# Kernel tuning notes

Measured on AMD Instinct MI355X. Metric: run time of the kernel, lower is better.

Reference implementation:

```python
import jax, jax.numpy as jnp
import numpy as np

DIM = 1024
HEADS = 16
HEAD_DIM = DIM // HEADS  # 64


def get_rope_matrix(seq_len: int, dim: int) -> jnp.ndarray:
    # rope[s, d] = concat(cos(s * inv_freq), sin(s * inv_freq))  -> (seq_len, dim)
    half = dim // 2
    inv_freq = 1.0 / (10000.0 ** (jnp.arange(half, dtype=jnp.float32) / half))
    sinusoid = jnp.arange(seq_len, dtype=jnp.float32)[:, None] * inv_freq[None, :]
    return jnp.concatenate([jnp.cos(sinusoid), jnp.sin(sinusoid)], axis=-1)


def setup_inputs() -> dict:
    key = jax.random.key(0)
    ks = jax.random.split(key, 6)
    B, T, D = 2, 2048, DIM
    scale = 1.0 / np.sqrt(D)
    return {
        "x": jax.random.normal(ks[0], (B, T, D), dtype=jnp.float32),
        "Wq": jax.random.normal(ks[1], (D, D), dtype=jnp.float32) * scale,
        "Wk": jax.random.normal(ks[2], (D, D), dtype=jnp.float32) * scale,
        "Wv": jax.random.normal(ks[3], (D, D), dtype=jnp.float32) * scale,
        "Wo": jax.random.normal(ks[4], (D, D), dtype=jnp.float32) * scale,
        "bo": jax.random.normal(ks[5], (D,), dtype=jnp.float32) * 0.01,
    }


def reference(x, Wq, Wk, Wv, Wo, bo):
    B, T, D = x.shape
    H, hd = HEADS, HEAD_DIM

    # projections -> (B, H, T, hd)
    def split_heads(y):
        return y.reshape(B, T, H, hd).transpose(0, 2, 1, 3)

    q = split_heads(x @ Wq)
    k = split_heads(x @ Wk)
    v = split_heads(x @ Wv)

    rope = get_rope_matrix(T, hd)  # (T, hd)

    # apply_rope(v, rope): einsum('...nd,sd->...ns') contracts head_dim -> (B,H,T,T)
    v_r = jnp.einsum('bhnd,sd->bhns', v, rope)

    scores = jax.nn.softmax(jnp.einsum('bhnd,bhmd->bhnm', q, k) / jnp.sqrt(jnp.float32(hd)), axis=-1)
    out = jnp.einsum('bhnm,bhms->bhns', scores, v_r)  # (B,H,T,T)

    # apply_rope(out, rope.T): out2[...,n,s] = sum_t out[...,n,t] * rope[t,s] -> (B,H,T,hd)
    out = jnp.einsum('bhnt,ts->bhns', out, rope)

    out = out.transpose(0, 2, 1, 3).reshape(B, T, D)
    return out @ Wo + bo
```

## Files before the change

kernel.cpp:

```cpp
#include <hip/hip_runtime.h>
#include <math.h>

#define DIM 1024
#define NH 16
#define HD 64
#define TT 2048
#define NTOK 4096

typedef __bf16 bf8v __attribute__((ext_vector_type(8)));
typedef float f4v __attribute__((ext_vector_type(4)));
typedef float f16v __attribute__((ext_vector_type(16)));
typedef unsigned short us8 __attribute__((ext_vector_type(8)));
typedef unsigned short us4 __attribute__((ext_vector_type(4)));
typedef unsigned int u4v __attribute__((ext_vector_type(4)));

static __device__ __forceinline__ unsigned short f2bf(float f) {
    unsigned int u = __float_as_uint(f);
    u += 0x7FFFu + ((u >> 16) & 1u);
    return (unsigned short)(u >> 16);
}
static __device__ __forceinline__ bf8v ld8(const unsigned short* p) {
    return __builtin_bit_cast(bf8v, *(const us8*)p);
}
static __device__ __forceinline__ void gl_lds(const unsigned short* g, unsigned short* l) {
    __builtin_amdgcn_global_load_lds((const __attribute__((address_space(1))) unsigned int*)(g),
                                     (__attribute__((address_space(3))) unsigned int*)(l), 16, 0, 0);
}

__global__ void k_prep(const float* __restrict__ x, unsigned short* __restrict__ xb,
                       const float* __restrict__ Wq, const float* __restrict__ Wk,
                       const float* __restrict__ Wv, unsigned short* __restrict__ wt,
                       float* __restrict__ rope, float* __restrict__ Rm) {
    int tid = threadIdx.x;
    int bb = blockIdx.x;
    if (bb < 4096) {
        int i = bb * 256 + tid;
        float4 v = ((const float4*)x)[i];
        us4 o;
        o[0] = f2bf(v.x); o[1] = f2bf(v.y); o[2] = f2bf(v.z); o[3] = f2bf(v.w);
        *(us4*)&xb[i * 4] = o;
    } else if (bb < 7168) {
        __shared__ float tile[32][33];
        bb -= 4096;
        int z = bb >> 10, rem = bb & 1023;
        int bx = rem & 31, by = rem >> 5;
        const float* W = (z == 0) ? Wq : ((z == 1) ? Wk : Wv);
        int tx = tid & 31, ty = tid >> 5;
        int c0 = bx * 32, k0 = by * 32;
#pragma unroll
        for (int j = 0; j < 4; j++)
            tile[ty + j * 8][tx] = W[(k0 + ty + j * 8) * DIM + c0 + tx];
        __syncthreads();
        unsigned short* out = wt + z * DIM * DIM;
#pragma unroll
        for (int j = 0; j < 4; j++)
            out[(c0 + ty + j * 8) * DIM + k0 + tx] = f2bf(tile[tx][ty + j * 8]);
    } else if (bb < 7680) {
        int i = (bb - 7168) * 256 + tid;
        int s = i >> 6, d = i & 63;
        float inv = exp2f(-(float)(d & 31) * (13.287712379549449f / 32.0f));
        float a = (float)s * inv;
        rope[i] = (d < 32) ? cosf(a) : sinf(a);
    } else {
        Rm[(bb - 7680) * 256 + tid] = 0.f;
    }
}

__global__ void k_R(const float* __restrict__ rope, float* __restrict__ R) {
    __shared__ float red[256];
    int d = blockIdx.x & 63, sg = blockIdx.x >> 6;
    int e = threadIdx.x & 63, sl = threadIdx.x >> 6;
    const float* rp = rope + (sg * 256 + sl * 64) * 64;
    float acc = 0.f;
    for (int s = 0; s < 64; s++)
        acc += rp[s * 64 + d] * rp[s * 64 + e];
    red[threadIdx.x] = acc;
    __syncthreads();
    if (sl == 0)
        atomicAdd(&R[d * 64 + e], (red[e] + red[e + 64]) + (red[e + 128] + red[e + 192]));
}

__global__ void k_wo2(const float* __restrict__ Wo, const float* __restrict__ R,
                      unsigned short* __restrict__ wo2t) {
    __shared__ float Ws[64 * 65];
    __shared__ float Rt[64 * 65];
    int tid = threadIdx.x;
    int h = blockIdx.y, j0 = blockIdx.x * 64;
    for (int idx = tid; idx < 4096; idx += 256) {
        int e = idx >> 6, j = idx & 63;
        Ws[e * 65 + j] = Wo[(h * 64 + e) * DIM + j0 + j];
        Rt[e * 65 + j] = R[j * 64 + e];
    }
    __syncthreads();
    int d = tid & 63, jb = (tid >> 6) * 16;
    float acc[16] = {};
    for (int e = 0; e < 64; e++) {
        float r = Rt[e * 65 + d];
#pragma unroll
        for (int jj = 0; jj < 16; jj++)
            acc[jj] += r * Ws[e * 65 + jb + jj];
    }
#pragma unroll
    for (int jj = 0; jj < 16; jj++)
        wo2t[(j0 + jb + jj) * DIM + h * 64 + d] = f2bf(acc[jj]);
}


__global__ __launch_bounds__(256, 3) void k_gemm_qkv(const unsigned short* __restrict__ A,
                                                     const unsigned short* __restrict__ Bt,
                                                     unsigned short* __restrict__ qk,
                                                     unsigned short* __restrict__ vt) {
    __shared__ unsigned short As[128 * 32];
    __shared__ unsigned short Bs[128 * 32];
    const int K = 1024;
    int tid = threadIdx.x;
    int lane = tid & 63, w = tid >> 6;
    int quad = lane >> 4, l16 = lane & 15;
    int m0 = blockIdx.y * 128, n0 = blockIdx.x * 128;
    int wm = (w >> 1) * 64, wn = (w & 1) * 64;

    int s0 = tid, s1 = 256 + tid;
    int r0 = s0 >> 2, cc0 = ((s0 & 3) ^ (r0 & 3)) * 8;
    int r1 = s1 >> 2, cc1 = ((s1 & 3) ^ (r1 & 3)) * 8;
    const unsigned short* Ag0 = A + (m0 + r0) * K + cc0;
    const unsigned short* Ag1 = A + (m0 + r1) * K + cc1;
    const unsigned short* Bg0 = Bt + (n0 + r0) * K + cc0;
    const unsigned short* Bg1 = Bt + (n0 + r1) * K + cc1;
    int qx = quad ^ (l16 & 3);

    f4v acc[4][4] = {};
    for (int k0 = 0; k0 < K; k0 += 32) {
        __syncthreads();
        gl_lds(Ag0 + k0, &As[s0 * 8]);
        gl_lds(Ag1 + k0, &As[s1 * 8]);
        gl_lds(Bg0 + k0, &Bs[s0 * 8]);
        gl_lds(Bg1 + k0, &Bs[s1 * 8]);
        __syncthreads();
        bf8v af[4], bf[4];
#pragma unroll
        for (int mt = 0; mt < 4; mt++)
            af[mt] = ld8(&As[(wm + mt * 16 + l16) * 32 + qx * 8]);
#pragma unroll
        for (int nt = 0; nt < 4; nt++)
            bf[nt] = ld8(&Bs[(wn + nt * 16 + l16) * 32 + qx * 8]);
#pragma unroll
        for (int mt = 0; mt < 4; mt++)
#pragma unroll
            for (int nt = 0; nt < 4; nt++)
                acc[mt][nt] = __builtin_amdgcn_mfma_f32_16x16x32_bf16(af[mt], bf[nt], acc[mt][nt], 0, 0, 0);
    }
#pragma unroll
    for (int mt = 0; mt < 4; mt++) {
#pragma unroll
        for (int nt = 0; nt < 4; nt++) {
            int gc = n0 + wn + nt * 16 + l16;
            int h = (gc >> 6) & 15;
            int d = gc & 63;
            if (gc < 2048) {
                float qs = (gc < 1024) ? 0.18033688011111793f : 1.0f;
                int mtx = gc >> 10;
                unsigned short* base = qk + mtx * (NTOK * DIM);
#pragma unroll
                for (int r = 0; r < 4; r++) {
                    int gm = m0 + wm + mt * 16 + quad * 4 + r;
                    int b = gm >> 11, t = gm & 2047;
                    base[((b * NH + h) * TT + t) * HD + d] = f2bf(acc[mt][nt][r] * qs);
                }
            } else {
                int gm0 = m0 + wm + mt * 16 + quad * 4;
                int b = gm0 >> 11, t = gm0 & 2047;
                us4 ov;
#pragma unroll
                for (int r = 0; r < 4; r++)
                    ov[r] = f2bf(acc[mt][nt][r]);
                *(us4*)&vt[(((b * NH + h) * HD) + d) * TT + t] = ov;
            }
        }
    }
}

__global__ __launch_bounds__(256, 2) void k_gemm_out(const unsigned short* __restrict__ A,
                                                     const unsigned short* __restrict__ Bt,
                                                     const float* __restrict__ bo,
                                                     float* __restrict__ out) {
    __shared__ unsigned short As[64 * 32];
    __shared__ unsigned short Bs[128 * 32];
    const int K = 1024;
    int tid = threadIdx.x;
    int lane = tid & 63, w = tid >> 6;
    int quad = lane >> 4, l16 = lane & 15;
    int bid = blockIdx.x;
    int xcd = bid & 7, slot = bid >> 3;
    int y = xcd * 8 + (slot & 7);
    int x = slot >> 3;
    int m0 = y * 64, n0 = x * 128;
    int wn = w * 32;

    int rr = tid >> 2, cc = ((tid & 3) ^ (rr & 3)) * 8;
    const unsigned short* Ag0 = A + (m0 + rr) * K + cc;
    const unsigned short* Bg0 = Bt + (n0 + rr) * K + cc;
    const unsigned short* Bg1 = Bt + (n0 + 64 + rr) * K + cc;
    int qx = quad ^ (l16 & 3);

    f4v acc[4][2] = {};
    for (int k0 = 0; k0 < K; k0 += 32) {
        __syncthreads();
        gl_lds(Ag0 + k0, &As[tid * 8]);
        gl_lds(Bg0 + k0, &Bs[tid * 8]);
        gl_lds(Bg1 + k0, &Bs[(256 + tid) * 8]);
        __syncthreads();
        bf8v af[4], bf[2];
#pragma unroll
        for (int mt = 0; mt < 4; mt++)
            af[mt] = ld8(&As[(mt * 16 + l16) * 32 + qx * 8]);
#pragma unroll
        for (int nt = 0; nt < 2; nt++)
            bf[nt] = ld8(&Bs[(wn + nt * 16 + l16) * 32 + qx * 8]);
#pragma unroll
        for (int mt = 0; mt < 4; mt++)
#pragma unroll
            for (int nt = 0; nt < 2; nt++)
                acc[mt][nt] = __builtin_amdgcn_mfma_f32_16x16x32_bf16(af[mt], bf[nt], acc[mt][nt], 0, 0, 0);
    }
#pragma unroll
    for (int mt = 0; mt < 4; mt++) {
#pragma unroll
        for (int nt = 0; nt < 2; nt++) {
            int gc = n0 + wn + nt * 16 + l16;
            float bias = bo[gc];
#pragma unroll
            for (int r = 0; r < 4; r++) {
                int gm = m0 + mt * 16 + quad * 4 + r;
                out[gm * DIM + gc] = acc[mt][nt][r] + bias;
            }
        }
    }
}

__global__ __launch_bounds__(256, 2) void k_flash(const unsigned short* __restrict__ qk,
                                                  const unsigned short* __restrict__ vt,
                                                  unsigned short* __restrict__ attn) {
    __shared__ unsigned short Ks[2][64 * 64];
    __shared__ unsigned short Vs[2][64 * 64];
    int tid = threadIdx.x;
    int lane = tid & 63, w = tid >> 6;
    int q31 = lane & 31, hi = lane >> 5;
    int bid = blockIdx.x;
    int xcd = bid & 7, sl = bid >> 3;
    int bh = xcd * 4 + (sl & 3);
    int qt = sl >> 2;

    const unsigned short* Qg = qk + bh * (TT * HD);
    const unsigned short* Kg = qk + NTOK * DIM + bh * (TT * HD);
    const unsigned short* Vg = vt + bh * (HD * TT);

    int qrow = qt * 128 + w * 32 + q31;
    bf8v qf[4];
#pragma unroll
    for (int ks = 0; ks < 4; ks++)
        qf[ks] = ld8(Qg + qrow * HD + ks * 16 + hi * 8);

    int r0 = tid >> 3, sw = (tid & 7) ^ (r0 & 7);
    int offK0 = r0 * HD + sw * 8, offK1 = offK0 + 32 * HD;
    int offV0 = r0 * TT + sw * 8, offV1 = offV0 + 32 * TT;
    int dst0 = tid * 8, dst1 = dst0 + 2048;

#define STAGE(tile, bufsel) do {                                  \
        const unsigned short* kb_ = Kg + (tile) * 64 * HD;        \
        const unsigned short* vb_ = Vg + (tile) * 64;             \
        gl_lds(kb_ + offK0, &Ks[bufsel][dst0]);                   \
        gl_lds(kb_ + offK1, &Ks[bufsel][dst1]);                   \
        gl_lds(vb_ + offV0, &Vs[bufsel][dst0]);                   \
        gl_lds(vb_ + offV1, &Vs[bufsel][dst1]);                   \
    } while (0)

    STAGE(0, 0);
    STAGE(1, 1);

    f16v oacc[2] = {};
    float lsg = 0.f;
    int xsw = q31 & 7;

    for (int it = 0; it < 32; it++) {
        int cur = it & 1;
        if (it == 31) { asm volatile("s_waitcnt vmcnt(0)" ::: "memory"); }
        else          { asm volatile("s_waitcnt vmcnt(4)" ::: "memory"); }
        __builtin_amdgcn_s_barrier();
        asm volatile("" ::: "memory");

        const unsigned short* Kb = Ks[cur];
        const unsigned short* Vb = Vs[cur];

        bf8v kf0[4], kf1[4];
#pragma unroll
        for (int ks = 0; ks < 4; ks++) {
            kf0[ks] = ld8(&Kb[(q31) * 64 + ((2 * ks + hi) ^ xsw) * 8]);
            kf1[ks] = ld8(&Kb[(32 + q31) * 64 + ((2 * ks + hi) ^ xsw) * 8]);
        }
        f16v s0 = {}, s1 = {};
#pragma unroll
        for (int ks = 0; ks < 4; ks++) {
            s0 = __builtin_amdgcn_mfma_f32_32x32x16_bf16(kf0[ks], qf[ks], s0, 0, 0, 0);
            s1 = __builtin_amdgcn_mfma_f32_32x32x16_bf16(kf1[ks], qf[ks], s1, 0, 0, 0);
        }

        bf8v vf[2][4];
#pragma unroll
        for (int kk = 0; kk < 4; kk++) {
            vf[0][kk] = ld8(&Vb[(q31) * 64 + ((2 * kk + hi) ^ xsw) * 8]);
            vf[1][kk] = ld8(&Vb[(32 + q31) * 64 + ((2 * kk + hi) ^ xsw) * 8]);
        }

#pragma unroll
        for (int mt = 0; mt < 2; mt++) {
#pragma unroll
            for (int sub = 0; sub < 2; sub++) {
                const f16v& s = mt ? s1 : s0;
                float pe[8];
#pragma unroll
                for (int j = 0; j < 8; j++)
                    pe[j] = __builtin_amdgcn_exp2f(s[sub * 8 + j]);
                float t01 = pe[0] + pe[1], t23 = pe[2] + pe[3];
                float t45 = pe[4] + pe[5], t67 = pe[6] + pe[7];
                lsg += (t01 + t23) + (t45 + t67);
                unsigned int e0, e1, e2, e3;
                asm("v_cvt_pk_bf16_f32 %0, %1, %2" : "=v"(e0) : "v"(pe[0]), "v"(pe[1]));
                asm("v_cvt_pk_bf16_f32 %0, %1, %2" : "=v"(e1) : "v"(pe[2]), "v"(pe[3]));
                asm("v_cvt_pk_bf16_f32 %0, %1, %2" : "=v"(e2) : "v"(pe[4]), "v"(pe[5]));
                asm("v_cvt_pk_bf16_f32 %0, %1, %2" : "=v"(e3) : "v"(pe[6]), "v"(pe[7]));
                asm("v_permlane32_swap_b32 %0, %1" : "+v"(e0), "+v"(e2));
                asm("v_permlane32_swap_b32 %0, %1" : "+v"(e1), "+v"(e3));
                u4v pv = {e0, e1, e2, e3};
                bf8v pb = __builtin_bit_cast(bf8v, pv);
                int kk = mt * 2 + sub;
                oacc[0] = __builtin_amdgcn_mfma_f32_32x32x16_bf16(vf[0][kk], pb, oacc[0], 0, 0, 0);
                oacc[1] = __builtin_amdgcn_mfma_f32_32x32x16_bf16(vf[1][kk], pb, oacc[1], 0, 0, 0);
            }
        }

        __builtin_amdgcn_s_barrier();
        asm volatile("" ::: "memory");
        if (it < 30) STAGE(it + 2, cur);
    }
#undef STAGE

    float lsum = lsg + __shfl_xor(lsg, 32, 64);
    float inv = __builtin_amdgcn_rcpf(lsum);
    int b = bh >> 4, h = bh & 15;
    unsigned short* dst = attn + ((b * TT) + qrow) * DIM + h * HD + hi * 4;
#pragma unroll
    for (int mtd = 0; mtd < 2; mtd++) {
#pragma unroll
        for (int g4 = 0; g4 < 4; g4++) {
            us4 ov;
#pragma unroll
            for (int r = 0; r < 4; r++)
                ov[r] = f2bf(oacc[mtd][g4 * 4 + r] * inv);
            *(us4*)&dst[mtd * 32 + g4 * 8] = ov;
        }
    }
}

extern "C" void kernel_launch(void* const* d_in, const int* in_sizes, int n_in,
                              void* d_out, int out_size, void* d_ws, size_t ws_size,
                              hipStream_t stream) {
    const float* x  = (const float*)d_in[0];
    const float* Wq = (const float*)d_in[1];
    const float* Wk = (const float*)d_in[2];
    const float* Wv = (const float*)d_in[3];
    const float* Wo = (const float*)d_in[4];
    const float* bo = (const float*)d_in[5];
    float* out = (float*)d_out;
    char* ws = (char*)d_ws;

    unsigned short* Xb    = (unsigned short*)(ws);
    unsigned short* Wqkvt = (unsigned short*)(ws + 8388608);
    unsigned short* attn  = (unsigned short*)(ws);
    unsigned short* QK    = (unsigned short*)(ws + 16777216);
    unsigned short* Vt    = (unsigned short*)(ws + 33554432);
    unsigned short* Wo2t  = (unsigned short*)(ws + 50331648);
    float*          rope  = (float*)(ws + 52428800);
    float*          Rm    = (float*)(ws + 52953088);

    hipLaunchKernelGGL(k_prep,     dim3(7696),   dim3(256), 0, stream, x, Xb, Wq, Wk, Wv, Wqkvt, rope, Rm);
    hipLaunchKernelGGL(k_R,        dim3(512),    dim3(256), 0, stream, rope, Rm);
    hipLaunchKernelGGL(k_wo2,      dim3(16, 16), dim3(256), 0, stream, Wo, Rm, Wo2t);
    hipLaunchKernelGGL(k_gemm_qkv, dim3(24, 32), dim3(256), 0, stream, Xb, Wqkvt, QK, Vt);
    hipLaunchKernelGGL(k_flash,    dim3(512),    dim3(256), 0, stream, QK, Vt, attn);
    hipLaunchKernelGGL(k_gemm_out, dim3(512),    dim3(256), 0, stream, attn, Wo2t, bo, out);
}
```

Baseline: 190.2 us.

## Split flash attention KV tiles across wave pairs with LDS reduction

New measurement: 196.9 us. +3.5%, slower.

```diff
diff --git a/kernel.cpp b/kernel.cpp
--- a/kernel.cpp
+++ b/kernel.cpp
@@ -237,7 +237,7 @@
     }
 }
 
-__global__ __launch_bounds__(256, 2) void k_flash(const unsigned short* __restrict__ qk,
+__global__ __launch_bounds__(256, 4) void k_flash(const unsigned short* __restrict__ qk,
                                                   const unsigned short* __restrict__ vt,
                                                   unsigned short* __restrict__ attn) {
     __shared__ unsigned short Ks[2][64 * 64];
@@ -245,6 +245,7 @@
     int tid = threadIdx.x;
     int lane = tid & 63, w = tid >> 6;
     int q31 = lane & 31, hi = lane >> 5;
+    int g = w >> 1, kh = w & 1;
     int bid = blockIdx.x;
     int xcd = bid & 7, sl = bid >> 3;
     int bh = xcd * 4 + (sl & 3);
@@ -254,7 +255,7 @@
     const unsigned short* Kg = qk + NTOK * DIM + bh * (TT * HD);
     const unsigned short* Vg = vt + bh * (HD * TT);
 
-    int qrow = qt * 128 + w * 32 + q31;
+    int qrow = qt * 64 + g * 32 + q31;
     bf8v qf[4];
 #pragma unroll
     for (int ks = 0; ks < 4; ks++)
@@ -280,6 +281,7 @@
     f16v oacc[2] = {};
     float lsg = 0.f;
     int xsw = q31 & 7;
+    int krow = kh * 32 + q31;
 
     for (int it = 0; it < 32; it++) {
         int cur = it & 1;
@@ -291,51 +293,43 @@
         const unsigned short* Kb = Ks[cur];
         const unsigned short* Vb = Vs[cur];
 
-        bf8v kf0[4], kf1[4];
-#pragma unroll
-        for (int ks = 0; ks < 4; ks++) {
-            kf0[ks] = ld8(&Kb[(q31) * 64 + ((2 * ks + hi) ^ xsw) * 8]);
-            kf1[ks] = ld8(&Kb[(32 + q31) * 64 + ((2 * ks + hi) ^ xsw) * 8]);
+        bf8v kf[4];
+#pragma unroll
+        for (int ks = 0; ks < 4; ks++)
+            kf[ks] = ld8(&Kb[krow * 64 + ((2 * ks + hi) ^ xsw) * 8]);
+        f16v s0 = {};
+#pragma unroll
+        for (int ks = 0; ks < 4; ks++)
+            s0 = __builtin_amdgcn_mfma_f32_32x32x16_bf16(kf[ks], qf[ks], s0, 0, 0, 0);
+
+        bf8v vf[2][2];
+#pragma unroll
+        for (int c = 0; c < 2; c++) {
+            int kkc = kh * 2 + c;
+            vf[0][c] = ld8(&Vb[(q31) * 64 + ((2 * kkc + hi) ^ xsw) * 8]);
+            vf[1][c] = ld8(&Vb[(32 + q31) * 64 + ((2 * kkc + hi) ^ xsw) * 8]);
         }
-        f16v s0 = {}, s1 = {};
-#pragma unroll
-        for (int ks = 0; ks < 4; ks++) {
-            s0 = __builtin_amdgcn_mfma_f32_32x32x16_bf16(kf0[ks], qf[ks], s0, 0, 0, 0);
-            s1 = __builtin_amdgcn_mfma_f32_32x32x16_bf16(kf1[ks], qf[ks], s1, 0, 0, 0);
-        }
-
-        bf8v vf[2][4];
-#pragma unroll
-        for (int kk = 0; kk < 4; kk++) {
-            vf[0][kk] = ld8(&Vb[(q31) * 64 + ((2 * kk + hi) ^ xsw) * 8]);
-            vf[1][kk] = ld8(&Vb[(32 + q31) * 64 + ((2 * kk + hi) ^ xsw) * 8]);
-        }
-
-#pragma unroll
-        for (int mt = 0; mt < 2; mt++) {
-#pragma unroll
-            for (int sub = 0; sub < 2; sub++) {
-                const f16v& s = mt ? s1 : s0;
-                float pe[8];
-#pragma unroll
-                for (int j = 0; j < 8; j++)
-                    pe[j] = __builtin_amdgcn_exp2f(s[sub * 8 + j]);
-                float t01 = pe[0] + pe[1], t23 = pe[2] + pe[3];
-                float t45 = pe[4] + pe[5], t67 = pe[6] + pe[7];
-                lsg += (t01 + t23) + (t45 + t67);
-                unsigned int e0, e1, e2, e3;
-                asm("v_cvt_pk_bf16_f32 %0, %1, %2" : "=v"(e0) : "v"(pe[0]), "v"(pe[1]));
-                asm("v_cvt_pk_bf16_f32 %0, %1, %2" : "=v"(e1) : "v"(pe[2]), "v"(pe[3]));
-                asm("v_cvt_pk_bf16_f32 %0, %1, %2" : "=v"(e2) : "v"(pe[4]), "v"(pe[5]));
-                asm("v_cvt_pk_bf16_f32 %0, %1, %2" : "=v"(e3) : "v"(pe[6]), "v"(pe[7]));
-                asm("v_permlane32_swap_b32 %0, %1" : "+v"(e0), "+v"(e2));
-                asm("v_permlane32_swap_b32 %0, %1" : "+v"(e1), "+v"(e3));
-                u4v pv = {e0, e1, e2, e3};
-                bf8v pb = __builtin_bit_cast(bf8v, pv);
-                int kk = mt * 2 + sub;
-                oacc[0] = __builtin_amdgcn_mfma_f32_32x32x16_bf16(vf[0][kk], pb, oacc[0], 0, 0, 0);
-                oacc[1] = __builtin_amdgcn_mfma_f32_32x32x16_bf16(vf[1][kk], pb, oacc[1], 0, 0, 0);
-            }
+
+#pragma unroll
+        for (int sub = 0; sub < 2; sub++) {
+            float pe[8];
+#pragma unroll
+            for (int j = 0; j < 8; j++)
+                pe[j] = __builtin_amdgcn_exp2f(s0[sub * 8 + j]);
+            float t01 = pe[0] + pe[1], t23 = pe[2] + pe[3];
+            float t45 = pe[4] + pe[5], t67 = pe[6] + pe[7];
+            lsg += (t01 + t23) + (t45 + t67);
+            unsigned int e0, e1, e2, e3;
+            asm("v_cvt_pk_bf16_f32 %0, %1, %2" : "=v"(e0) : "v"(pe[0]), "v"(pe[1]));
+            asm("v_cvt_pk_bf16_f32 %0, %1, %2" : "=v"(e1) : "v"(pe[2]), "v"(pe[3]));
+            asm("v_cvt_pk_bf16_f32 %0, %1, %2" : "=v"(e2) : "v"(pe[4]), "v"(pe[5]));
+            asm("v_cvt_pk_bf16_f32 %0, %1, %2" : "=v"(e3) : "v"(pe[6]), "v"(pe[7]));
+            asm("v_permlane32_swap_b32 %0, %1" : "+v"(e0), "+v"(e2));
+            asm("v_permlane32_swap_b32 %0, %1" : "+v"(e1), "+v"(e3));
+            u4v pv = {e0, e1, e2, e3};
+            bf8v pb = __builtin_bit_cast(bf8v, pv);
+            oacc[0] = __builtin_amdgcn_mfma_f32_32x32x16_bf16(vf[0][sub], pb, oacc[0], 0, 0, 0);
+            oacc[1] = __builtin_amdgcn_mfma_f32_32x32x16_bf16(vf[1][sub], pb, oacc[1], 0, 0, 0);
         }
 
         __builtin_amdgcn_s_barrier();
@@ -345,18 +339,37 @@
 #undef STAGE
 
     float lsum = lsg + __shfl_xor(lsg, 32, 64);
-    float inv = __builtin_amdgcn_rcpf(lsum);
-    int b = bh >> 4, h = bh & 15;
-    unsigned short* dst = attn + ((b * TT) + qrow) * DIM + h * HD + hi * 4;
-#pragma unroll
-    for (int mtd = 0; mtd < 2; mtd++) {
-#pragma unroll
-        for (int g4 = 0; g4 < 4; g4++) {
-            us4 ov;
-#pragma unroll
-            for (int r = 0; r < 4; r++)
-                ov[r] = f2bf(oacc[mtd][g4 * 4 + r] * inv);
-            *(us4*)&dst[mtd * 32 + g4 * 8] = ov;
+    float* redo = (float*)&Ks[0][0];
+    float* redl = (float*)&Vs[0][0];
+    if (kh == 1) {
+#pragma unroll
+        for (int mtd = 0; mtd < 2; mtd++)
+#pragma unroll
+            for (int j = 0; j < 16; j++)
+                redo[g * 2048 + (mtd * 16 + j) * 64 + lane] = oacc[mtd][j];
+        redl[g * 64 + lane] = lsum;
+    }
+    __syncthreads();
+    if (kh == 0) {
+#pragma unroll
+        for (int mtd = 0; mtd < 2; mtd++)
+#pragma unroll
+            for (int j = 0; j < 16; j++)
+                oacc[mtd][j] += redo[g * 2048 + (mtd * 16 + j) * 64 + lane];
+        lsum += redl[g * 64 + lane];
+        float inv = __builtin_amdgcn_rcpf(lsum);
+        int b = bh >> 4, h = bh & 15;
+        unsigned short* dst = attn + ((b * TT) + qrow) * DIM + h * HD + hi * 4;
+#pragma unroll
+        for (int mtd = 0; mtd < 2; mtd++) {
+#pragma unroll
+            for (int g4 = 0; g4 < 4; g4++) {
+                us4 ov;
+#pragma unroll
+                for (int r = 0; r < 4; r++)
+                    ov[r] = f2bf(oacc[mtd][g4 * 4 + r] * inv);
+                *(us4*)&dst[mtd * 32 + g4 * 8] = ov;
+            }
         }
     }
 }
@@ -386,6 +399,6 @@
     hipLaunchKernelGGL(k_R,        dim3(512),    dim3(256), 0, stream, rope, Rm);
     hipLaunchKernelGGL(k_wo2,      dim3(16, 16), dim3(256), 0, stream, Wo, Rm, Wo2t);
     hipLaunchKernelGGL(k_gemm_qkv, dim3(24, 32), dim3(256), 0, stream, Xb, Wqkvt, QK, Vt);
-    hipLaunchKernelGGL(k_flash,    dim3(512),    dim3(256), 0, stream, QK, Vt, attn);
+    hipLaunchKernelGGL(k_flash,    dim3(1024),   dim3(256), 0, stream, QK, Vt, attn);
     hipLaunchKernelGGL(k_gemm_out, dim3(512),    dim3(256), 0, stream, attn, Wo2t, bo, out);
 }
```

## Double-buffer LDS tiles in QKV GEMM with async prefetch two stages ahead

Applied to the files above, without the earlier changes.

After: 190.7 us. About the same (+0.2%).

```diff
diff --git a/kernel.cpp b/kernel.cpp
--- a/kernel.cpp
+++ b/kernel.cpp
@@ -110,8 +110,8 @@
                                                      const unsigned short* __restrict__ Bt,
                                                      unsigned short* __restrict__ qk,
                                                      unsigned short* __restrict__ vt) {
-    __shared__ unsigned short As[128 * 32];
-    __shared__ unsigned short Bs[128 * 32];
+    __shared__ unsigned short As[2][128 * 32];
+    __shared__ unsigned short Bs[2][128 * 32];
     const int K = 1024;
     int tid = threadIdx.x;
     int lane = tid & 63, w = tid >> 6;
@@ -128,27 +128,41 @@
     const unsigned short* Bg1 = Bt + (n0 + r1) * K + cc1;
     int qx = quad ^ (l16 & 3);
 
+#define QSTAGE(t, buf) do {                                 \
+        int kk_ = (t) * 32;                                 \
+        gl_lds(Ag0 + kk_, &As[buf][s0 * 8]);                \
+        gl_lds(Ag1 + kk_, &As[buf][s1 * 8]);                \
+        gl_lds(Bg0 + kk_, &Bs[buf][s0 * 8]);                \
+        gl_lds(Bg1 + kk_, &Bs[buf][s1 * 8]);                \
+    } while (0)
+
+    QSTAGE(0, 0);
+    QSTAGE(1, 1);
+
     f4v acc[4][4] = {};
-    for (int k0 = 0; k0 < K; k0 += 32) {
-        __syncthreads();
-        gl_lds(Ag0 + k0, &As[s0 * 8]);
-        gl_lds(Ag1 + k0, &As[s1 * 8]);
-        gl_lds(Bg0 + k0, &Bs[s0 * 8]);
-        gl_lds(Bg1 + k0, &Bs[s1 * 8]);
-        __syncthreads();
+    for (int it = 0; it < 32; it++) {
+        int cur = it & 1;
+        if (it == 31) { asm volatile("s_waitcnt vmcnt(0)" ::: "memory"); }
+        else          { asm volatile("s_waitcnt vmcnt(4)" ::: "memory"); }
+        __builtin_amdgcn_s_barrier();
+        asm volatile("" ::: "memory");
         bf8v af[4], bf[4];
 #pragma unroll
         for (int mt = 0; mt < 4; mt++)
-            af[mt] = ld8(&As[(wm + mt * 16 + l16) * 32 + qx * 8]);
+            af[mt] = ld8(&As[cur][(wm + mt * 16 + l16) * 32 + qx * 8]);
 #pragma unroll
         for (int nt = 0; nt < 4; nt++)
-            bf[nt] = ld8(&Bs[(wn + nt * 16 + l16) * 32 + qx * 8]);
+            bf[nt] = ld8(&Bs[cur][(wn + nt * 16 + l16) * 32 + qx * 8]);
 #pragma unroll
         for (int mt = 0; mt < 4; mt++)
 #pragma unroll
             for (int nt = 0; nt < 4; nt++)
                 acc[mt][nt] = __builtin_amdgcn_mfma_f32_16x16x32_bf16(af[mt], bf[nt], acc[mt][nt], 0, 0, 0);
-    }
+        __builtin_amdgcn_s_barrier();
+        asm volatile("" ::: "memory");
+        if (it < 30) QSTAGE(it + 2, cur);
+    }
+#undef QSTAGE
 #pragma unroll
     for (int mt = 0; mt < 4; mt++) {
 #pragma unroll
```
